# Optimization experiments

Hardware: AMD Instinct MI355X
Metric: run time of the kernel (lower is better)

## Reference

```python
import jax, jax.numpy as jnp
import numpy as np
import math

D_MODEL = 768
NUM_HEADS = 12
HEAD_DIM = D_MODEL // NUM_HEADS
HIDDEN = 3072
EPS = 1e-05
CLAMP = 1e9


def setup_inputs() -> dict:
    key = jax.random.key(0)
    ks = jax.random.split(key, 8)
    s = 0.02
    return {
        "x": jax.random.normal(ks[0], (1, 4096, D_MODEL), dtype=jnp.float32),
        "gamma1": jnp.ones((D_MODEL,), jnp.float32),
        "beta1": jnp.zeros((D_MODEL,), jnp.float32),
        "Wqkv": jax.random.normal(ks[1], (D_MODEL, 3 * D_MODEL), jnp.float32) * s,
        "bqkv": jnp.zeros((3 * D_MODEL,), jnp.float32),
        "Wo": jax.random.normal(ks[2], (D_MODEL, D_MODEL), jnp.float32) * s,
        "bo": jnp.zeros((D_MODEL,), jnp.float32),
        "gamma2": jnp.ones((D_MODEL,), jnp.float32),
        "beta2": jnp.zeros((D_MODEL,), jnp.float32),
        "W1": jax.random.normal(ks[3], (D_MODEL, HIDDEN), jnp.float32) * s,
        "b1": jnp.zeros((HIDDEN,), jnp.float32),
        "W2": jax.random.normal(ks[4], (HIDDEN, D_MODEL), jnp.float32) * s,
        "b2": jnp.zeros((D_MODEL,), jnp.float32),
    }


def layer_norm(x, gamma, beta):
    mean = jnp.mean(x, axis=-1, keepdims=True)
    var = jnp.mean((x - mean) ** 2, axis=-1, keepdims=True)
    y = (x - mean) / jnp.sqrt(var + EPS)
    return gamma * y + beta


def attention_block(x, Wqkv, bqkv, Wo, bo):
    B, S, D = x.shape
    qkv = x @ Wqkv + bqkv                             # [B,S,3D]
    qkv = qkv.reshape(B, S, NUM_HEADS, 3 * HEAD_DIM).transpose(0, 2, 1, 3)  # [B,H,S,3hd]
    q, k, v = jnp.split(qkv, 3, axis=-1)              # each [B,H,S,hd]
    scaled = jnp.einsum("bhqd,bhkd->bhqk", q, k) / math.sqrt(HEAD_DIM)
    causal = jnp.tril(jnp.ones((S, S), dtype=bool))
    scaled = jnp.where(causal, scaled, -jnp.inf)
    scaled = jnp.clip(scaled, -CLAMP, CLAMP)          # torch clamp turns -inf into -1e9
    attn = jax.nn.softmax(scaled, axis=-1)
    vals = jnp.einsum("bhqk,bhkd->bhqd", attn, v)     # [B,H,S,hd]
    vals = vals.transpose(0, 2, 1, 3).reshape(B, S, D)
    return vals @ Wo + bo


def ffn_block(x, W1, b1, W2, b2):
    h = jax.nn.gelu(x @ W1 + b1, approximate=False)
    return h @ W2 + b2


def reference(x, gamma1, beta1, Wqkv, bqkv, Wo, bo, gamma2, beta2, W1, b1, W2, b2):
    x = x + attention_block(layer_norm(x, gamma1, beta1), Wqkv, bqkv, Wo, bo)
    x = x + ffn_block(layer_norm(x, gamma2, beta2), W1, b1, W2, b2)
    return x
```

## Files before the change

kernel.cpp:

```cpp
#include <hip/hip_runtime.h>
#include <hip/hip_bf16.h>
#include <cmath>

using u16 = unsigned short;
typedef __bf16 bf16x8 __attribute__((ext_vector_type(8)));
typedef __bf16 bf16x2 __attribute__((ext_vector_type(2)));
typedef unsigned short u16x8 __attribute__((ext_vector_type(8)));
typedef float f32x4 __attribute__((ext_vector_type(4)));

#define SEQ 4096
#define DM 768
#define NH 12
#define HD 64
#define HID 3072

__device__ __forceinline__ u16 f2bf(float f) {
    union { float f; unsigned u; } v; v.f = f;
    unsigned r = v.u + 0x7fffu + ((v.u >> 16) & 1u);
    return (u16)(r >> 16);
}

__device__ __forceinline__ unsigned pack_bf16(float a, float b) {
    union { bf16x2 v; unsigned u; } c;
    c.v[0] = (__bf16)a; c.v[1] = (__bf16)b;
    return c.u;
}

__device__ __forceinline__ int swz64(int row, int k) {
    return (row << 6) | ((((k >> 3) ^ row) & 7) << 3) | (k & 7);
}
__device__ __forceinline__ int swz128(int row, int k) {
    return (row << 7) | ((((k >> 3) ^ row) & 15) << 3) | (k & 7);
}

__global__ void transpose_to_bf16(const float* __restrict__ W, u16* __restrict__ Wt,
                                  int K, int N) {
    __shared__ float tile[32][33];
    int kb = blockIdx.y * 32, nb = blockIdx.x * 32;
    int tx = threadIdx.x, ty = threadIdx.y;
#pragma unroll
    for (int i = 0; i < 32; i += 8)
        tile[ty + i][tx] = W[(size_t)(kb + ty + i) * N + nb + tx];
    __syncthreads();
#pragma unroll
    for (int i = 0; i < 32; i += 8)
        Wt[(size_t)(nb + ty + i) * K + kb + tx] = f2bf(tile[tx][ty + i]);
}

__global__ __launch_bounds__(256) void ln_kernel(const float* __restrict__ x,
                                                 const float* __restrict__ g,
                                                 const float* __restrict__ b,
                                                 u16* __restrict__ y) {
    int row = blockIdx.x, t = threadIdx.x;
    const float* xr = x + (size_t)row * DM;
    float v0 = xr[t], v1 = xr[t + 256], v2 = xr[t + 512];
    float s = v0 + v1 + v2;
#pragma unroll
    for (int m = 32; m; m >>= 1) s += __shfl_xor(s, m);
    __shared__ float red[4], red2[4];
    int wid = t >> 6, lane = t & 63;
    if (lane == 0) red[wid] = s;
    __syncthreads();
    float mean = (red[0] + red[1] + red[2] + red[3]) * (1.0f / DM);
    float d0 = v0 - mean, d1 = v1 - mean, d2 = v2 - mean;
    float q = d0 * d0 + d1 * d1 + d2 * d2;
#pragma unroll
    for (int m = 32; m; m >>= 1) q += __shfl_xor(q, m);
    if (lane == 0) red2[wid] = q;
    __syncthreads();
    float var = (red2[0] + red2[1] + red2[2] + red2[3]) * (1.0f / DM);
    float rstd = rsqrtf(var + 1e-5f);
    y[(size_t)row * DM + t]       = f2bf(d0 * rstd * g[t]       + b[t]);
    y[(size_t)row * DM + t + 256] = f2bf(d1 * rstd * g[t + 256] + b[t + 256]);
    y[(size_t)row * DM + t + 512] = f2bf(d2 * rstd * g[t + 512] + b[t + 512]);
}

template<int TM>
__global__ __launch_bounds__(256) void gemm_bf16(
    const u16* __restrict__ A, const u16* __restrict__ Bt,
    const float* __restrict__ bias, const float* __restrict__ resid,
    float* __restrict__ outF, u16* __restrict__ outB,
    int M, int N, int K, int gelu) {
    constexpr int AP = TM / 32;
    constexpr int NF = (TM == 128) ? 4 : 2;
    __shared__ __align__(16) u16 As[TM * 64];
    __shared__ __align__(16) u16 Bs[128 * 64];
    int tid = threadIdx.x;
    int lane = tid & 63, wid = tid >> 6;
    int lr = lane & 15, hi = lane >> 4;
    int wrow = (TM == 128) ? (wid >> 1) * 64 : 0;
    int wcol = (TM == 128) ? (wid & 1) * 64 : wid * 32;
    int m0 = blockIdx.y * TM, n0 = blockIdx.x * 128;

    f32x4 acc[4][NF] = {};
    int srow = tid >> 3;
    int sk = (tid & 7) << 3;
    const u16* Ag = A + (size_t)(m0 + srow) * K + sk;
    const u16* Bg = Bt + (size_t)(n0 + srow) * K + sk;

    for (int kt = 0; kt < K; kt += 64) {
        u16x8 ar[AP], br[4];
#pragma unroll
        for (int p = 0; p < AP; ++p)
            ar[p] = *reinterpret_cast<const u16x8*>(Ag + (size_t)p * 32 * K + kt);
#pragma unroll
        for (int p = 0; p < 4; ++p)
            br[p] = *reinterpret_cast<const u16x8*>(Bg + (size_t)p * 32 * K + kt);
        __syncthreads();
#pragma unroll
        for (int p = 0; p < AP; ++p)
            *reinterpret_cast<u16x8*>(&As[swz64(srow + p * 32, sk)]) = ar[p];
#pragma unroll
        for (int p = 0; p < 4; ++p)
            *reinterpret_cast<u16x8*>(&Bs[swz64(srow + p * 32, sk)]) = br[p];
        __syncthreads();
#pragma unroll
        for (int ks = 0; ks < 2; ++ks) {
            bf16x8 af[4], bfr[NF];
#pragma unroll
            for (int m = 0; m < 4; ++m)
                af[m] = *reinterpret_cast<const bf16x8*>(&As[swz64(wrow + m * 16 + lr, ks * 32 + hi * 8)]);
#pragma unroll
            for (int n = 0; n < NF; ++n)
                bfr[n] = *reinterpret_cast<const bf16x8*>(&Bs[swz64(wcol + n * 16 + lr, ks * 32 + hi * 8)]);
            __builtin_amdgcn_s_setprio(1);
#pragma unroll
            for (int m = 0; m < 4; ++m)
#pragma unroll
                for (int n = 0; n < NF; ++n)
                    acc[m][n] = __builtin_amdgcn_mfma_f32_16x16x32_bf16(af[m], bfr[n], acc[m][n], 0, 0, 0);
            __builtin_amdgcn_s_setprio(0);
        }
    }
#pragma unroll
    for (int m = 0; m < 4; ++m) {
#pragma unroll
        for (int n = 0; n < NF; ++n) {
            int col = n0 + wcol + n * 16 + lr;
            float bv = bias[col];
#pragma unroll
            for (int r = 0; r < 4; ++r) {
                int row = m0 + wrow + m * 16 + hi * 4 + r;
                float v = acc[m][n][r] + bv;
                if (gelu) v = 0.5f * v * (1.0f + erff(v * 0.70710678118654752f));
                if (resid) v += resid[(size_t)row * N + col];
                if (outF) outF[(size_t)row * N + col] = v;
                if (outB) outB[(size_t)row * N + col] = f2bf(v);
            }
        }
    }
}

__global__ __launch_bounds__(256, 3) void attn_kernel(const u16* __restrict__ qkv,
                                                      u16* __restrict__ attn) {
    __shared__ __align__(16) u16 Ks[128 * 64];
    __shared__ __align__(16) u16 Vt[64 * 128];
    int tid = threadIdx.x;
    int lane = tid & 63, w = tid >> 6;
    int lr = lane & 15, hi = lane >> 4;
    int upper = hi >> 1;
    const float SCL = 0.125f * 1.44269504088896340736f;

    int bid = blockIdx.x;
    int h = bid % NH;
    int qb = (SEQ / 64 - 1) - bid / NH;

    int qrow = qb * 64 + w * 16 + lr;
    bf16x8 qf[2];
#pragma unroll
    for (int ks = 0; ks < 2; ++ks)
        qf[ks] = *reinterpret_cast<const bf16x8*>(&qkv[(size_t)qrow * 2304 + h * 192 + ks * 32 + hi * 8]);

    f32x4 acc[4] = {};
    float m_run = -INFINITY, l_run = 0.0f;

    int nt = (qb * 64 + 64 + 127) >> 7;
    for (int kb = 0; kb < nt; ++kb) {
        __syncthreads();
#pragma unroll
        for (int p = 0; p < 4; ++p) {
            int kvr = (tid >> 3) + p * 32;
            int c = (tid & 7) << 3;
            u16x8 kv = *reinterpret_cast<const u16x8*>(
                &qkv[(size_t)(kb * 128 + kvr) * 2304 + h * 192 + 64 + c]);
            *reinterpret_cast<u16x8*>(&Ks[swz64(kvr, c)]) = kv;
        }
        {
            int d = tid & 63;
            int kvq = (tid >> 6) * 32;
            const u16* vb = &qkv[(size_t)(kb * 128 + kvq) * 2304 + h * 192 + 128 + d];
#pragma unroll
            for (int g = 0; g < 4; ++g) {
                u16x8 vv;
#pragma unroll
                for (int j = 0; j < 8; ++j)
                    vv[j] = vb[(size_t)(g * 8 + j) * 2304];
                *reinterpret_cast<u16x8*>(&Vt[swz128(d, kvq + g * 8)]) = vv;
            }
        }
        __syncthreads();

        f32x4 s[8] = {};
        __builtin_amdgcn_s_setprio(1);
#pragma unroll
        for (int ks = 0; ks < 2; ++ks) {
#pragma unroll
            for (int n = 0; n < 8; ++n) {
                bf16x8 kf = *reinterpret_cast<const bf16x8*>(&Ks[swz64(n * 16 + lr, ks * 32 + hi * 8)]);
                s[n] = __builtin_amdgcn_mfma_f32_16x16x32_bf16(kf, qf[ks], s[n], 0, 0, 0);
            }
        }
        __builtin_amdgcn_s_setprio(0);
        float sv[8][4];
#pragma unroll
        for (int n = 0; n < 8; ++n) {
            sv[n][0] = s[n][0]; sv[n][1] = s[n][1]; sv[n][2] = s[n][2]; sv[n][3] = s[n][3];
        }
        if (kb == nt - 1) {
#pragma unroll
            for (int n = 0; n < 8; ++n)
#pragma unroll
                for (int r = 0; r < 4; ++r) {
                    int kv = kb * 128 + n * 16 + hi * 4 + r;
                    if (kv > qrow) sv[n][r] = -3.0e38f;
                }
        }
        float t8[8];
#pragma unroll
        for (int n = 0; n < 8; ++n)
            t8[n] = fmaxf(fmaxf(sv[n][0], sv[n][1]), fmaxf(sv[n][2], sv[n][3]));
        float mx = fmaxf(fmaxf(fmaxf(t8[0], t8[1]), fmaxf(t8[2], t8[3])),
                         fmaxf(fmaxf(t8[4], t8[5]), fmaxf(t8[6], t8[7])));
        mx = fmaxf(mx, __shfl_xor(mx, 16));
        mx = fmaxf(mx, __shfl_xor(mx, 32));
        float mnew = fmaxf(m_run, mx * SCL);
        float alpha = __builtin_amdgcn_exp2f(m_run - mnew);
        float rs = 0.0f;
#pragma unroll
        for (int n = 0; n < 8; ++n) {
            float p0 = __builtin_amdgcn_exp2f(__builtin_fmaf(sv[n][0], SCL, -mnew));
            float p1 = __builtin_amdgcn_exp2f(__builtin_fmaf(sv[n][1], SCL, -mnew));
            float p2 = __builtin_amdgcn_exp2f(__builtin_fmaf(sv[n][2], SCL, -mnew));
            float p3 = __builtin_amdgcn_exp2f(__builtin_fmaf(sv[n][3], SCL, -mnew));
            sv[n][0] = p0; sv[n][1] = p1; sv[n][2] = p2; sv[n][3] = p3;
            rs += (p0 + p1) + (p2 + p3);
        }
        rs += __shfl_xor(rs, 16);
        rs += __shfl_xor(rs, 32);
        l_run = l_run * alpha + rs;
        m_run = mnew;
#pragma unroll
        for (int n2 = 0; n2 < 4; ++n2)
#pragma unroll
            for (int r = 0; r < 4; ++r) acc[n2][r] *= alpha;

        unsigned pk0[8], pk1[8];
#pragma unroll
        for (int n = 0; n < 8; ++n) {
            pk0[n] = pack_bf16(sv[n][0], sv[n][1]);
            pk1[n] = pack_bf16(sv[n][2], sv[n][3]);
        }
        int src0 = lr + ((hi & 1) << 5);
        int src1 = src0 + 16;
#pragma unroll
        for (int ks = 0; ks < 4; ++ks) {
            union { unsigned w4[4]; bf16x8 v; } pf;
            {
                unsigned a0 = __shfl(pk0[2 * ks], src0), b0 = __shfl(pk0[2 * ks + 1], src0);
                unsigned a1 = __shfl(pk1[2 * ks], src0), b1 = __shfl(pk1[2 * ks + 1], src0);
                unsigned a2 = __shfl(pk0[2 * ks], src1), b2 = __shfl(pk0[2 * ks + 1], src1);
                unsigned a3 = __shfl(pk1[2 * ks], src1), b3 = __shfl(pk1[2 * ks + 1], src1);
                pf.w4[0] = upper ? b0 : a0;
                pf.w4[1] = upper ? b1 : a1;
                pf.w4[2] = upper ? b2 : a2;
                pf.w4[3] = upper ? b3 : a3;
            }
            __builtin_amdgcn_s_setprio(1);
#pragma unroll
            for (int n2 = 0; n2 < 4; ++n2) {
                bf16x8 vf = *reinterpret_cast<const bf16x8*>(&Vt[swz128(n2 * 16 + lr, ks * 32 + hi * 8)]);
                acc[n2] = __builtin_amdgcn_mfma_f32_16x16x32_bf16(vf, pf.v, acc[n2], 0, 0, 0);
            }
            __builtin_amdgcn_s_setprio(0);
        }
    }
    float inv = 1.0f / l_run;
#pragma unroll
    for (int n2 = 0; n2 < 4; ++n2) {
#pragma unroll
        for (int r = 0; r < 4; ++r) {
            int dcol = h * 64 + n2 * 16 + hi * 4 + r;
            attn[(size_t)qrow * DM + dcol] = f2bf(acc[n2][r] * inv);
        }
    }
}

extern "C" void kernel_launch(void* const* d_in, const int* in_sizes, int n_in,
                              void* d_out, int out_size, void* d_ws, size_t ws_size,
                              hipStream_t stream) {
    const float* x      = (const float*)d_in[0];
    const float* gamma1 = (const float*)d_in[1];
    const float* beta1  = (const float*)d_in[2];
    const float* Wqkv   = (const float*)d_in[3];
    const float* bqkv   = (const float*)d_in[4];
    const float* Wo     = (const float*)d_in[5];
    const float* bo     = (const float*)d_in[6];
    const float* gamma2 = (const float*)d_in[7];
    const float* beta2  = (const float*)d_in[8];
    const float* W1     = (const float*)d_in[9];
    const float* b1     = (const float*)d_in[10];
    const float* W2     = (const float*)d_in[11];
    const float* b2     = (const float*)d_in[12];

    char* ws = (char*)d_ws;
    size_t off = 0;
    u16* WqkvT = (u16*)(ws + off); off += (size_t)2304 * 768 * 2;
    u16* WoT   = (u16*)(ws + off); off += (size_t)768 * 768 * 2;
    u16* W1T   = (u16*)(ws + off); off += (size_t)3072 * 768 * 2;
    u16* W2T   = (u16*)(ws + off); off += (size_t)768 * 3072 * 2;
    u16* B1    = (u16*)(ws + off); off += (size_t)SEQ * DM * 2;
    u16* Q     = (u16*)(ws + off); off += (size_t)SEQ * HID * 2;
    float* x1  = (float*)(ws + off); off += (size_t)SEQ * DM * 4;

    dim3 tb(32, 8);
    transpose_to_bf16<<<dim3(2304 / 32, 768 / 32), tb, 0, stream>>>(Wqkv, WqkvT, 768, 2304);
    transpose_to_bf16<<<dim3(768 / 32, 768 / 32), tb, 0, stream>>>(Wo, WoT, 768, 768);
    transpose_to_bf16<<<dim3(3072 / 32, 768 / 32), tb, 0, stream>>>(W1, W1T, 768, 3072);
    transpose_to_bf16<<<dim3(768 / 32, 3072 / 32), tb, 0, stream>>>(W2, W2T, 3072, 768);

    ln_kernel<<<SEQ, 256, 0, stream>>>(x, gamma1, beta1, B1);
    gemm_bf16<128><<<dim3(2304 / 128, SEQ / 128), 256, 0, stream>>>(B1, WqkvT, bqkv, nullptr, nullptr, Q, SEQ, 2304, 768, 0);
    attn_kernel<<<dim3((SEQ / 64) * NH), 256, 0, stream>>>(Q, B1);
    gemm_bf16<64><<<dim3(768 / 128, SEQ / 64), 256, 0, stream>>>(B1, WoT, bo, x, x1, nullptr, SEQ, 768, 768, 0);
    ln_kernel<<<SEQ, 256, 0, stream>>>(x1, gamma2, beta2, B1);
    gemm_bf16<128><<<dim3(3072 / 128, SEQ / 128), 256, 0, stream>>>(B1, W1T, b1, nullptr, nullptr, Q, SEQ, 3072, 768, 1);
    gemm_bf16<64><<<dim3(768 / 128, SEQ / 64), 256, 0, stream>>>(Q, W2T, b2, x1, (float*)d_out, nullptr, SEQ, 768, 3072, 0);
}
```

Measured before the change: 257.4 us.

## Double-buffer GEMM tiles with direct global-to-LDS loads and faster GELU

The bf16 GEMM now stages A and B tiles straight from global memory into swizzled LDS with global_load_lds, instead of going through registers. Two LDS buffers let the load of the next K-tile overlap the MFMA work on the current one, and one barrier per iteration replaces two. The epilogue's erff-based GELU is swapped for an Abramowitz-Stegun polynomial built on hardware rcp and exp2, which trims the cost of the GELU epilogue. In exchange, LDS use doubles, which may lower occupancy, and correctness depends on the barrier waiting for the asynchronous LDS writes to finish.

Measured after the change: 262.1 us. About the same (+1.8%).

```diff
diff --git a/kernel.cpp b/kernel.cpp
--- a/kernel.cpp
+++ b/kernel.cpp
@@ -14,6 +14,10 @@
 #define HD 64
 #define HID 3072
 
+#define GLD_LDS16(g, l) __builtin_amdgcn_global_load_lds( \
+    (const __attribute__((address_space(1))) void*)(g),   \
+    (__attribute__((address_space(3))) void*)(l), 16, 0, 0)
+
 __device__ __forceinline__ u16 f2bf(float f) {
     union { float f; unsigned u; } v; v.f = f;
     unsigned r = v.u + 0x7fffu + ((v.u >> 16) & 1u);
@@ -24,6 +28,18 @@
     union { bf16x2 v; unsigned u; } c;
     c.v[0] = (__bf16)a; c.v[1] = (__bf16)b;
     return c.u;
+}
+
+__device__ __forceinline__ float gelu_exact(float v) {
+    float z = fabsf(v) * 0.70710678118654752f;
+    float t = __builtin_amdgcn_rcpf(__builtin_fmaf(0.3275911f, z, 1.0f));
+    float p = t * __builtin_fmaf(t, __builtin_fmaf(t, __builtin_fmaf(t,
+                __builtin_fmaf(t, 1.061405429f, -1.453152027f),
+                1.421413741f), -0.284496736f), 0.254829592f);
+    float e = __builtin_amdgcn_exp2f(-z * z * 1.44269504088896341f);
+    float erfv = __builtin_fmaf(-p, e, 1.0f);
+    erfv = (v < 0.0f) ? -erfv : erfv;
+    return 0.5f * v * (1.0f + erfv);
 }
 
 __device__ __forceinline__ int swz64(int row, int k) {
@@ -83,8 +99,8 @@
     int M, int N, int K, int gelu) {
     constexpr int AP = TM / 32;
     constexpr int NF = (TM == 128) ? 4 : 2;
-    __shared__ __align__(16) u16 As[TM * 64];
-    __shared__ __align__(16) u16 Bs[128 * 64];
+    __shared__ __align__(16) u16 As[2][TM * 64];
+    __shared__ __align__(16) u16 Bs[2][128 * 64];
     int tid = threadIdx.x;
     int lane = tid & 63, wid = tid >> 6;
     int lr = lane & 15, hi = lane >> 4;
@@ -93,36 +109,41 @@
     int m0 = blockIdx.y * TM, n0 = blockIdx.x * 128;
 
     f32x4 acc[4][NF] = {};
-    int srow = tid >> 3;
-    int sk = (tid & 7) << 3;
-    const u16* Ag = A + (size_t)(m0 + srow) * K + sk;
-    const u16* Bg = Bt + (size_t)(n0 + srow) * K + sk;
-
-    for (int kt = 0; kt < K; kt += 64) {
-        u16x8 ar[AP], br[4];
-#pragma unroll
-        for (int p = 0; p < AP; ++p)
-            ar[p] = *reinterpret_cast<const u16x8*>(Ag + (size_t)p * 32 * K + kt);
-#pragma unroll
-        for (int p = 0; p < 4; ++p)
-            br[p] = *reinterpret_cast<const u16x8*>(Bg + (size_t)p * 32 * K + kt);
+    int rsub = wid * 8 + (lane >> 3);
+    int chunk = lane & 7;
+
+    auto STAGE = [&](int buf, int kt) {
+#pragma unroll
+        for (int p = 0; p < AP; ++p) {
+            int row = p * 32 + rsub;
+            int col = kt + (((chunk ^ row) & 7) << 3);
+            GLD_LDS16(A + (size_t)(m0 + row) * K + col, &As[buf][(p * 32 + wid * 8) * 64]);
+        }
+#pragma unroll
+        for (int p = 0; p < 4; ++p) {
+            int row = p * 32 + rsub;
+            int col = kt + (((chunk ^ row) & 7) << 3);
+            GLD_LDS16(Bt + (size_t)(n0 + row) * K + col, &Bs[buf][(p * 32 + wid * 8) * 64]);
+        }
+    };
+
+    int NT = K >> 6;
+    STAGE(0, 0);
+#pragma unroll 2
+    for (int t = 0; t < NT; ++t) {
         __syncthreads();
-#pragma unroll
-        for (int p = 0; p < AP; ++p)
-            *reinterpret_cast<u16x8*>(&As[swz64(srow + p * 32, sk)]) = ar[p];
-#pragma unroll
-        for (int p = 0; p < 4; ++p)
-            *reinterpret_cast<u16x8*>(&Bs[swz64(srow + p * 32, sk)]) = br[p];
-        __syncthreads();
+        if (t + 1 < NT) STAGE((t + 1) & 1, (t + 1) << 6);
+        const u16* as = &As[t & 1][0];
+        const u16* bs = &Bs[t & 1][0];
 #pragma unroll
         for (int ks = 0; ks < 2; ++ks) {
             bf16x8 af[4], bfr[NF];
 #pragma unroll
             for (int m = 0; m < 4; ++m)
-                af[m] = *reinterpret_cast<const bf16x8*>(&As[swz64(wrow + m * 16 + lr, ks * 32 + hi * 8)]);
+                af[m] = *reinterpret_cast<const bf16x8*>(&as[swz64(wrow + m * 16 + lr, ks * 32 + hi * 8)]);
 #pragma unroll
             for (int n = 0; n < NF; ++n)
-                bfr[n] = *reinterpret_cast<const bf16x8*>(&Bs[swz64(wcol + n * 16 + lr, ks * 32 + hi * 8)]);
+                bfr[n] = *reinterpret_cast<const bf16x8*>(&bs[swz64(wcol + n * 16 + lr, ks * 32 + hi * 8)]);
             __builtin_amdgcn_s_setprio(1);
 #pragma unroll
             for (int m = 0; m < 4; ++m)
@@ -142,7 +163,7 @@
             for (int r = 0; r < 4; ++r) {
                 int row = m0 + wrow + m * 16 + hi * 4 + r;
                 float v = acc[m][n][r] + bv;
-                if (gelu) v = 0.5f * v * (1.0f + erff(v * 0.70710678118654752f));
+                if (gelu) v = gelu_exact(v);
                 if (resid) v += resid[(size_t)row * N + col];
                 if (outF) outF[(size_t)row * N + col] = v;
                 if (outB) outB[(size_t)row * N + col] = f2bf(v);
```
